# Kernel tuning notes

Hardware: AMD Instinct MI355X
Metric: run time of the kernel (lower is better)

The kernel has to match this reference:

```python
import jax, jax.numpy as jnp
import numpy as np

N, E, IN_DIM, H, D = 50000, 800000, 64, 8, 8
HD = H * D
CLAMP = 5.0


def setup_inputs() -> dict:
    key = jax.random.key(0)
    ks = jax.random.split(key, 13)
    s_in = 1.0 / np.sqrt(IN_DIM)
    s_hd = 1.0 / np.sqrt(HD)
    return {
        "x": jax.random.normal(ks[0], (N, IN_DIM), jnp.float32),
        "edge_attr": jax.random.normal(ks[1], (E, IN_DIM), jnp.float32),
        "edge_index": jax.random.randint(ks[2], (2, E), 0, N, jnp.int32),
        # torch nn.Linear weights are [out_features, in_features]
        "WQ": jax.random.normal(ks[3], (HD, IN_DIM), jnp.float32) * s_in,
        "WK": jax.random.normal(ks[4], (HD, IN_DIM), jnp.float32) * s_in,
        "WV": jax.random.normal(ks[5], (HD, IN_DIM), jnp.float32) * s_in,
        "WEw": jax.random.normal(ks[6], (HD, IN_DIM), jnp.float32) * s_in,
        "WEb": jax.random.normal(ks[7], (HD, IN_DIM), jnp.float32) * s_in,
        "bEb": jax.random.normal(ks[8], (HD,), jnp.float32) * 0.02,
        "WEo": jax.random.normal(ks[9], (HD, HD), jnp.float32) * s_hd,
        "bEo": jax.random.normal(ks[10], (HD,), jnp.float32) * 0.02,
        "Aw": jax.random.normal(ks[11], (D, H, 1), jnp.float32) * s_hd,
        "BW": jax.random.normal(ks[12], (D, H, D), jnp.float32) * s_hd,
    }


def _scatter_softmax(score, dst, num_nodes):
    # score: [E, H, 1]; softmax over edges grouped by dst node
    mx = jax.ops.segment_max(score, dst, num_segments=num_nodes)  # [N,H,1]
    ex = jnp.exp(score - mx[dst])
    den = jax.ops.segment_sum(ex, dst, num_segments=num_nodes)    # [N,H,1]
    return ex / (den[dst] + 1e-16)


def reference(x, edge_attr, edge_index, WQ, WK, WV, WEw, WEb, bEb, WEo, bEo, Aw, BW):
    n = x.shape[0]
    e = edge_attr.shape[0]
    Qh = (x @ WQ.T).reshape(n, H, D)
    Kh = (x @ WK.T).reshape(n, H, D)
    Vh = (x @ WV.T).reshape(n, H, D)
    Ew = (edge_attr @ WEw.T).reshape(e, H, D)
    Eb = (edge_attr @ WEb.T + bEb).reshape(e, H, D)

    dst, src = edge_index[0], edge_index[1]
    conn1 = (Qh[dst] + Kh[src]) * Ew                       # [E,H,D]
    # sqrt(relu(x)) - sqrt(relu(-x)) == sign(x)*sqrt(|x|)
    conn2 = jnp.sign(conn1) * jnp.sqrt(jnp.abs(conn1))
    conn = conn2 + Eb                                      # act = Identity

    Eo_flat = conn.reshape(e, HD) @ WEo.T + bEo            # Oe output [E, H*D]
    Eo = Eo_flat.reshape(e, H, D)

    score = jnp.einsum('ehd,dhc->ehc', conn, Aw)           # [E,H,1]
    score = jnp.clip(score, -CLAMP, CLAMP)
    score = _scatter_softmax(score, dst, n)

    agg = jax.ops.segment_sum(Vh[src] * score, dst, num_segments=n)   # [N,H,D]
    rowV = jax.ops.segment_sum(Eo * score, dst, num_segments=n)       # [N,H,D]
    rowV = jnp.einsum('nhd,dhc->nhc', rowV, BW)
    h_out = agg + rowV                                     # [N,H,D]
    return (h_out, Eo_flat)
```

## Files before the change

kernel.cpp:

```cpp
#include <hip/hip_runtime.h>

#define NN 50000
#define EE 800000
#define NTILES (EE / 128)
#define NB ((NN + 1023) / 1024)

typedef __attribute__((ext_vector_type(8))) short short8;
typedef __attribute__((ext_vector_type(16))) float f32x16;
typedef unsigned short ushort_t;

static __device__ __forceinline__ unsigned short f2bf(float f) {
    unsigned u = __float_as_uint(f);
    u += 0x7fffu + ((u >> 16) & 1u);
    return (unsigned short)(u >> 16);
}
static __device__ __forceinline__ unsigned cvt_pk(float lo, float hi) {
    unsigned r;
    asm("v_cvt_pk_bf16_f32 %0, %1, %2" : "=v"(r) : "v"(lo), "v"(hi));
    return r;
}
static __device__ __forceinline__ float bf2f(unsigned short s) {
    return __uint_as_float((unsigned)s << 16);
}
static __device__ __forceinline__ float lo_f(unsigned u) { return __uint_as_float(u << 16); }
static __device__ __forceinline__ float hi_f(unsigned u) { return __uint_as_float(u & 0xffff0000u); }
static __device__ __forceinline__ f32x16 splat16(float v) {
    f32x16 r;
    #pragma unroll
    for (int i = 0; i < 16; ++i) r[i] = v;
    return r;
}

union U8 { short8 v; uint2 u[2]; };

static __device__ __forceinline__ short8 ldsfrag(const unsigned short* rowbase, int k0) {
    U8 t;
    t.u[0] = *(const uint2*)(rowbase + k0);
    t.u[1] = *(const uint2*)(rowbase + k0 + 8);
    return t.v;
}

__global__ __launch_bounds__(256) void qkv_mfma_kernel(
    const float* __restrict__ x,
    const float* __restrict__ WQ, const float* __restrict__ WK, const float* __restrict__ WV,
    ushort_t* __restrict__ Qb, ushort_t* __restrict__ Kb, ushort_t* __restrict__ Vb)
{
    __shared__ unsigned short s_wq[64][68];
    __shared__ unsigned short s_wk[64][68];
    __shared__ unsigned short s_wv[64][68];

    int tid = threadIdx.x;
    #pragma unroll
    for (int t = 0; t < 8; ++t) {
        int idx = (t * 256 + tid) * 2;
        int r = idx >> 6, c = idx & 63;
        float2 w = *(const float2*)(WQ + idx);
        *(unsigned*)&s_wq[r][c] = cvt_pk(w.x, w.y);
        w = *(const float2*)(WK + idx);
        *(unsigned*)&s_wk[r][c] = cvt_pk(w.x, w.y);
        w = *(const float2*)(WV + idx);
        *(unsigned*)&s_wv[r][c] = cvt_pk(w.x, w.y);
    }
    __syncthreads();

    int wid = tid >> 6, lane = tid & 63;
    int m0 = blockIdx.x * 128 + wid * 32;
    int lo5 = lane & 31, hi = lane >> 5;

    int rowi = m0 + lo5;
    const float* arow = x + (size_t)(rowi < NN ? rowi : NN - 1) * 64;
    short8 af[4];
    #pragma unroll
    for (int ks = 0; ks < 4; ++ks) {
        int k0 = ks * 16 + hi * 4;
        float4 a0 = *(const float4*)(arow + k0);
        float4 a1 = *(const float4*)(arow + k0 + 8);
        U8 t;
        t.u[0] = make_uint2(cvt_pk(a0.x, a0.y), cvt_pk(a0.z, a0.w));
        t.u[1] = make_uint2(cvt_pk(a1.x, a1.y), cvt_pk(a1.z, a1.w));
        af[ks] = t.v;
    }

    #pragma unroll
    for (int nt = 0; nt < 2; ++nt) {
        int n = nt * 32 + lo5;
        f32x16 cQ = splat16(0.f), cK = splat16(0.f), cV = splat16(0.f);
        #pragma unroll
        for (int ks = 0; ks < 4; ++ks) {
            int k0 = ks * 16 + hi * 4;
            cQ = __builtin_amdgcn_mfma_f32_32x32x16_bf16(af[ks], ldsfrag(s_wq[n], k0), cQ, 0, 0, 0);
            cK = __builtin_amdgcn_mfma_f32_32x32x16_bf16(af[ks], ldsfrag(s_wk[n], k0), cK, 0, 0, 0);
            cV = __builtin_amdgcn_mfma_f32_32x32x16_bf16(af[ks], ldsfrag(s_wv[n], k0), cV, 0, 0, 0);
        }
        #pragma unroll
        for (int r = 0; r < 16; ++r) {
            int m = (r & 3) + 8 * (r >> 2) + 4 * hi;
            int gm = m0 + m;
            if (gm < NN) {
                Qb[(size_t)gm * 64 + n] = (ushort_t)cvt_pk(cQ[r], cQ[r]);
                Kb[(size_t)gm * 64 + n] = (ushort_t)cvt_pk(cK[r], cK[r]);
                Vb[(size_t)gm * 64 + n] = (ushort_t)cvt_pk(cV[r], cV[r]);
            }
        }
    }
}

__global__ __launch_bounds__(256) void hist_kernel(const int* __restrict__ eidx,
                                                   int* __restrict__ cnt)
{
    int e = blockIdx.x * blockDim.x + threadIdx.x;
    atomicAdd(&cnt[eidx[e]], 1);
}

__global__ __launch_bounds__(1024) void scan1_kernel(const int* __restrict__ cnt,
                                                     int* __restrict__ rowstart,
                                                     int* __restrict__ bsum)
{
    __shared__ int buf[1024];
    int tid = threadIdx.x;
    int i = blockIdx.x * 1024 + tid;
    int v = (i < NN) ? cnt[i] : 0;
    buf[tid] = v;
    __syncthreads();
    for (int off = 1; off < 1024; off <<= 1) {
        int t = (tid >= off) ? buf[tid - off] : 0;
        __syncthreads();
        buf[tid] += t;
        __syncthreads();
    }
    if (i < NN) rowstart[i] = buf[tid] - v;
    if (tid == 1023) bsum[blockIdx.x] = buf[1023];
}

__global__ __launch_bounds__(64) void scan2_kernel(const int* __restrict__ bsum,
                                                   int* __restrict__ boff,
                                                   int* __restrict__ rowstart)
{
    int lane = threadIdx.x;
    int v = (lane < NB) ? bsum[lane] : 0;
    int s = v;
    #pragma unroll
    for (int off = 1; off < 64; off <<= 1) {
        int t = __shfl_up(s, off, 64);
        if (lane >= off) s += t;
    }
    if (lane < NB) boff[lane] = s - v;
    if (lane == 63) rowstart[NN] = s;
}

__global__ __launch_bounds__(1024) void scan3_kernel(int* __restrict__ rowstart,
                                                     const int* __restrict__ boff,
                                                     int* __restrict__ cursor)
{
    int i = blockIdx.x * 1024 + threadIdx.x;
    if (i < NN) {
        int r = rowstart[i] + boff[blockIdx.x];
        rowstart[i] = r;
        cursor[i] = r;
    }
}

__global__ __launch_bounds__(256) void scatter_kernel(const int* __restrict__ eidx,
                                                      int* __restrict__ cursor,
                                                      int2* __restrict__ edges_csr,
                                                      int* __restrict__ inv)
{
    int e = blockIdx.x * blockDim.x + threadIdx.x;
    int dst = eidx[e];
    int pos = atomicAdd(&cursor[dst], 1);
    edges_csr[pos] = make_int2(e, eidx[EE + e]);
    inv[e] = pos;
}

__global__ __launch_bounds__(256) void edge_mfma_kernel(
    const float* __restrict__ eattr, const int* __restrict__ eidx,
    const int* __restrict__ inv,
    const float* __restrict__ WEw, const float* __restrict__ WEb, const float* __restrict__ bEb,
    const float* __restrict__ WEo, const float* __restrict__ bEo, const float* __restrict__ Aw,
    const ushort_t* __restrict__ Qb, const ushort_t* __restrict__ Kb,
    float* __restrict__ Eo_out, float* __restrict__ exbuf)
{
    __shared__ unsigned short s_wew[64][68];
    __shared__ unsigned short s_web[64][68];
    __shared__ unsigned short s_weo[64][68];
    __shared__ unsigned short s_cq[4][32][68];

    int tid = threadIdx.x;
    #pragma unroll
    for (int t = 0; t < 8; ++t) {
        int idx = (t * 256 + tid) * 2;
        int r = idx >> 6, c = idx & 63;
        float2 w = *(const float2*)(WEw + idx);
        *(unsigned*)&s_wew[r][c] = cvt_pk(w.x, w.y);
        w = *(const float2*)(WEb + idx);
        *(unsigned*)&s_web[r][c] = cvt_pk(w.x, w.y);
        w = *(const float2*)(WEo + idx);
        *(unsigned*)&s_weo[r][c] = cvt_pk(w.x, w.y);
    }
    __syncthreads();

    int wid = tid >> 6, lane = tid & 63;
    int lo5 = lane & 31, hi = lane >> 5;
    int mm = lane >> 4;
    int cc = (lane & 15) * 4;

    float awv[32];
    #pragma unroll
    for (int ks = 0; ks < 4; ++ks)
        #pragma unroll
        for (int i = 0; i < 8; ++i) {
            int k = ks * 16 + hi * 4 + (i & 3) + ((i >> 2) << 3);
            awv[ks * 8 + i] = Aw[(k & 7) * 8 + (k >> 3)];
        }
    float bEbn0 = bEb[lo5], bEbn1 = bEb[32 + lo5];
    float bEon0 = bEo[lo5], bEon1 = bEo[32 + lo5];

    for (int tile = blockIdx.x; tile < NTILES; tile += gridDim.x) {
        int e0 = tile * 128 + wid * 32;
        int pos = inv[e0 + lo5];

        #pragma unroll
        for (int t = 0; t < 8; ++t) {
            int m = t * 4 + mm;
            int e = e0 + m;
            int dst = eidx[e], src = eidx[EE + e];
            uint2 q = *(const uint2*)(Qb + (size_t)dst * 64 + cc);
            uint2 k = *(const uint2*)(Kb + (size_t)src * 64 + cc);
            float s0 = lo_f(q.x) + lo_f(k.x);
            float s1 = hi_f(q.x) + hi_f(k.x);
            float s2 = lo_f(q.y) + lo_f(k.y);
            float s3 = hi_f(q.y) + hi_f(k.y);
            *(uint2*)&s_cq[wid][m][cc] = make_uint2(cvt_pk(s0, s1), cvt_pk(s2, s3));
        }

        short8 af[4];
        {
            const float* arow = eattr + (size_t)(e0 + lo5) * 64;
            #pragma unroll
            for (int ks = 0; ks < 4; ++ks) {
                int k0 = ks * 16 + hi * 4;
                float4 a0 = *(const float4*)(arow + k0);
                float4 a1 = *(const float4*)(arow + k0 + 8);
                U8 t;
                t.u[0] = make_uint2(cvt_pk(a0.x, a0.y), cvt_pk(a0.z, a0.w));
                t.u[1] = make_uint2(cvt_pk(a1.x, a1.y), cvt_pk(a1.z, a1.w));
                af[ks] = t.v;
            }
        }

        #pragma unroll
        for (int nt = 0; nt < 2; ++nt) {
            int n = nt * 32 + lo5;
            f32x16 cEw = splat16(0.f), cEb = splat16(0.f);
            #pragma unroll
            for (int ks = 0; ks < 4; ++ks) {
                int k0 = ks * 16 + hi * 4;
                cEw = __builtin_amdgcn_mfma_f32_32x32x16_bf16(af[ks], ldsfrag(s_wew[n], k0), cEw, 0, 0, 0);
                cEb = __builtin_amdgcn_mfma_f32_32x32x16_bf16(af[ks], ldsfrag(s_web[n], k0), cEb, 0, 0, 0);
            }
            float bEbn = nt ? bEbn1 : bEbn0;
            #pragma unroll
            for (int r = 0; r < 16; ++r) {
                int m = (r & 3) + 8 * (r >> 2) + 4 * hi;
                float qk = bf2f(s_cq[wid][m][n]);
                float c1 = qk * cEw[r];
                float c2 = copysignf(sqrtf(fabsf(c1)), c1);
                s_cq[wid][m][n] = f2bf(c2 + cEb[r] + bEbn);
            }
        }

        short8 ca[4];
        #pragma unroll
        for (int ks = 0; ks < 4; ++ks) {
            int k0 = ks * 16 + hi * 4;
            ca[ks] = ldsfrag(s_cq[wid][lo5], k0);
        }

        {
            float sc[8];
            #pragma unroll
            for (int h2 = 0; h2 < 8; ++h2) sc[h2] = 0.f;
            #pragma unroll
            for (int ks = 0; ks < 4; ++ks)
                #pragma unroll
                for (int i = 0; i < 8; ++i) {
                    float cv = bf2f((unsigned short)ca[ks][i]);
                    sc[2 * ks + (i >> 2)] = fmaf(cv, awv[ks * 8 + i], sc[2 * ks + (i >> 2)]);
                }
            #pragma unroll
            for (int h2 = 0; h2 < 8; ++h2) {
                sc[h2] += __shfl_xor(sc[h2], 32, 64);
                sc[h2] = fminf(fmaxf(sc[h2], -5.0f), 5.0f);
                sc[h2] = __expf(sc[h2]);
            }
            if (hi == 0) {
                *(float4*)(exbuf + (size_t)pos * 8 + 0) = make_float4(sc[0], sc[1], sc[2], sc[3]);
                *(float4*)(exbuf + (size_t)pos * 8 + 4) = make_float4(sc[4], sc[5], sc[6], sc[7]);
            }
        }

        #pragma unroll
        for (int nt = 0; nt < 2; ++nt) {
            int n = nt * 32 + lo5;
            f32x16 cO = splat16(nt ? bEon1 : bEon0);
            #pragma unroll
            for (int ks = 0; ks < 4; ++ks) {
                int k0 = ks * 16 + hi * 4;
                cO = __builtin_amdgcn_mfma_f32_32x32x16_bf16(ca[ks], ldsfrag(s_weo[n], k0), cO, 0, 0, 0);
            }
            #pragma unroll
            for (int r = 0; r < 16; ++r) {
                int m = (r & 3) + 8 * (r >> 2) + 4 * hi;
                Eo_out[(size_t)(e0 + m) * 64 + n] = cO[r];
            }
        }
    }
}

__global__ __launch_bounds__(256) void node_kernel(
    const int* __restrict__ rowstart, const int2* __restrict__ edges_csr,
    const float* __restrict__ exbuf, const float* __restrict__ Eo,
    const ushort_t* __restrict__ Vb, const float* __restrict__ BW,
    float* __restrict__ hout)
{
    int n = (blockIdx.x * blockDim.x + threadIdx.x) >> 6;
    int lane = threadIdx.x & 63;
    int h = lane >> 3, d = lane & 7;

    int beg = rowstart[n], end = rowstart[n + 1];
    float agg0 = 0.f, rv0 = 0.f, den0 = 0.f;
    float agg1 = 0.f, rv1 = 0.f, den1 = 0.f;
    int j = beg;
    for (; j + 3 < end; j += 4) {
        int2 p0 = edges_csr[j + 0];
        int2 p1 = edges_csr[j + 1];
        int2 p2 = edges_csr[j + 2];
        int2 p3 = edges_csr[j + 3];
        float x0 = exbuf[(size_t)(j + 0) * 8 + h];
        float x1 = exbuf[(size_t)(j + 1) * 8 + h];
        float x2 = exbuf[(size_t)(j + 2) * 8 + h];
        float x3 = exbuf[(size_t)(j + 3) * 8 + h];
        float v0 = bf2f(Vb[(size_t)p0.y * 64 + lane]);
        float o0 = Eo[(size_t)p0.x * 64 + lane];
        float v1 = bf2f(Vb[(size_t)p1.y * 64 + lane]);
        float o1 = Eo[(size_t)p1.x * 64 + lane];
        float v2 = bf2f(Vb[(size_t)p2.y * 64 + lane]);
        float o2 = Eo[(size_t)p2.x * 64 + lane];
        float v3 = bf2f(Vb[(size_t)p3.y * 64 + lane]);
        float o3 = Eo[(size_t)p3.x * 64 + lane];
        agg0 = fmaf(x0, v0, agg0); rv0 = fmaf(x0, o0, rv0); den0 += x0;
        agg1 = fmaf(x1, v1, agg1); rv1 = fmaf(x1, o1, rv1); den1 += x1;
        agg0 = fmaf(x2, v2, agg0); rv0 = fmaf(x2, o2, rv0); den0 += x2;
        agg1 = fmaf(x3, v3, agg1); rv1 = fmaf(x3, o3, rv1); den1 += x3;
    }
    for (; j < end; ++j) {
        int2 p0 = edges_csr[j];
        float x0 = exbuf[(size_t)j * 8 + h];
        agg0 = fmaf(x0, bf2f(Vb[(size_t)p0.y * 64 + lane]), agg0);
        rv0  = fmaf(x0, Eo[(size_t)p0.x * 64 + lane], rv0);
        den0 += x0;
    }
    float agg = agg0 + agg1, rv = rv0 + rv1, den = den0 + den1;
    float inv = (den > 0.f) ? (1.0f / den) : 0.f;

    float acc = agg;
    #pragma unroll
    for (int dd = 0; dd < 8; ++dd) {
        float rvd = __shfl(rv, (h << 3) + dd, 64);
        acc = fmaf(rvd, BW[dd * 64 + (h << 3) + d], acc);
    }
    hout[(size_t)n * 64 + lane] = acc * inv;
}

extern "C" void kernel_launch(void* const* d_in, const int* in_sizes, int n_in,
                              void* d_out, int out_size, void* d_ws, size_t ws_size,
                              hipStream_t stream)
{
    const float* x    = (const float*)d_in[0];
    const float* ea   = (const float*)d_in[1];
    const int*   eidx = (const int*)  d_in[2];
    const float* WQ   = (const float*)d_in[3];
    const float* WK   = (const float*)d_in[4];
    const float* WV   = (const float*)d_in[5];
    const float* WEw  = (const float*)d_in[6];
    const float* WEb  = (const float*)d_in[7];
    const float* bEb  = (const float*)d_in[8];
    const float* WEo  = (const float*)d_in[9];
    const float* bEo  = (const float*)d_in[10];
    const float* Aw   = (const float*)d_in[11];
    const float* BW   = (const float*)d_in[12];

    float* hout   = (float*)d_out;
    float* Eo_out = hout + (size_t)NN * 64;

    ushort_t* Qb = (ushort_t*)d_ws;
    ushort_t* Kb = Qb + (size_t)NN * 64;
    ushort_t* Vb = Kb + (size_t)NN * 64;
    float* exbuf = (float*)(Vb + (size_t)NN * 64);
    int* cnt      = (int*)(exbuf + (size_t)EE * 8);
    int* rowstart = cnt + NN;
    int2* edges_csr = (int2*)(rowstart + NN + 2);
    int* invp     = (int*)(edges_csr + EE);
    int* bsum     = invp + EE;
    int* boff     = bsum + 64;

    hipMemsetAsync(cnt, 0, (size_t)NN * sizeof(int), stream);

    hist_kernel<<<EE / 256, 256, 0, stream>>>(eidx, cnt);
    scan1_kernel<<<NB, 1024, 0, stream>>>(cnt, rowstart, bsum);
    scan2_kernel<<<1, 64, 0, stream>>>(bsum, boff, rowstart);
    scan3_kernel<<<NB, 1024, 0, stream>>>(rowstart, boff, cnt);
    scatter_kernel<<<EE / 256, 256, 0, stream>>>(eidx, cnt, edges_csr, invp);

    qkv_mfma_kernel<<<(NN + 127) / 128, 256, 0, stream>>>(x, WQ, WK, WV, Qb, Kb, Vb);

    edge_mfma_kernel<<<2080, 256, 0, stream>>>(ea, eidx, invp, WEw, WEb, bEb,
                                               WEo, bEo, Aw, Qb, Kb, Eo_out, exbuf);

    node_kernel<<<(NN * 64) / 256, 256, 0, stream>>>(rowstart, edges_csr,
                                                     exbuf, Eo_out, Vb, BW, hout);
}
```

Before: 318.7 us.

## Write bf16 Eo copy in CSR order so node kernel reads it contiguously

The edge kernel now also writes a bf16 copy of Eo, permuted into destination-sorted CSR order, into extra workspace. The node kernel then reads this copy contiguously instead of gathering fp32 Eo rows by edge id. The aim is to replace a random 256B-per-edge gather with a sequential 128B read. The cost is an extra scattered 2-byte-per-element write in the edge kernel, which is poorly coalesced, plus bf16 rounding in the rowV path. A fallback path is used when the workspace is too small, and there the node kernel's unroll drops from 4 to 2.

```diff
diff --git a/kernel.cpp b/kernel.cpp
--- a/kernel.cpp
+++ b/kernel.cpp
@@ -172,18 +172,21 @@
     inv[e] = pos;
 }
 
+template<bool WCSR>
 __global__ __launch_bounds__(256) void edge_mfma_kernel(
     const float* __restrict__ eattr, const int* __restrict__ eidx,
     const int* __restrict__ inv,
     const float* __restrict__ WEw, const float* __restrict__ WEb, const float* __restrict__ bEb,
     const float* __restrict__ WEo, const float* __restrict__ bEo, const float* __restrict__ Aw,
     const ushort_t* __restrict__ Qb, const ushort_t* __restrict__ Kb,
-    float* __restrict__ Eo_out, float* __restrict__ exbuf)
+    float* __restrict__ Eo_out, float* __restrict__ exbuf,
+    ushort_t* __restrict__ eocsr)
 {
     __shared__ unsigned short s_wew[64][68];
     __shared__ unsigned short s_web[64][68];
     __shared__ unsigned short s_weo[64][68];
     __shared__ unsigned short s_cq[4][32][68];
+    __shared__ int s_inv[4][32];
 
     int tid = threadIdx.x;
     #pragma unroll
@@ -218,6 +221,7 @@
     for (int tile = blockIdx.x; tile < NTILES; tile += gridDim.x) {
         int e0 = tile * 128 + wid * 32;
         int pos = inv[e0 + lo5];
+        if (WCSR) s_inv[wid][lo5] = pos;
 
         #pragma unroll
         for (int t = 0; t < 8; ++t) {
@@ -312,14 +316,18 @@
             for (int r = 0; r < 16; ++r) {
                 int m = (r & 3) + 8 * (r >> 2) + 4 * hi;
                 Eo_out[(size_t)(e0 + m) * 64 + n] = cO[r];
-            }
-        }
-    }
-}
-
-__global__ __launch_bounds__(256) void node_kernel(
+                if (WCSR) {
+                    int pm = s_inv[wid][m];
+                    eocsr[(size_t)pm * 64 + n] = (ushort_t)cvt_pk(cO[r], cO[r]);
+                }
+            }
+        }
+    }
+}
+
+__global__ __launch_bounds__(256) void node_kernel_csr(
     const int* __restrict__ rowstart, const int2* __restrict__ edges_csr,
-    const float* __restrict__ exbuf, const float* __restrict__ Eo,
+    const float* __restrict__ exbuf, const ushort_t* __restrict__ eocsr,
     const ushort_t* __restrict__ Vb, const float* __restrict__ BW,
     float* __restrict__ hout)
 {
@@ -341,19 +349,64 @@
         float x2 = exbuf[(size_t)(j + 2) * 8 + h];
         float x3 = exbuf[(size_t)(j + 3) * 8 + h];
         float v0 = bf2f(Vb[(size_t)p0.y * 64 + lane]);
-        float o0 = Eo[(size_t)p0.x * 64 + lane];
+        float o0 = bf2f(eocsr[(size_t)(j + 0) * 64 + lane]);
         float v1 = bf2f(Vb[(size_t)p1.y * 64 + lane]);
-        float o1 = Eo[(size_t)p1.x * 64 + lane];
+        float o1 = bf2f(eocsr[(size_t)(j + 1) * 64 + lane]);
         float v2 = bf2f(Vb[(size_t)p2.y * 64 + lane]);
-        float o2 = Eo[(size_t)p2.x * 64 + lane];
+        float o2 = bf2f(eocsr[(size_t)(j + 2) * 64 + lane]);
         float v3 = bf2f(Vb[(size_t)p3.y * 64 + lane]);
-        float o3 = Eo[(size_t)p3.x * 64 + lane];
+        float o3 = bf2f(eocsr[(size_t)(j + 3) * 64 + lane]);
         agg0 = fmaf(x0, v0, agg0); rv0 = fmaf(x0, o0, rv0); den0 += x0;
         agg1 = fmaf(x1, v1, agg1); rv1 = fmaf(x1, o1, rv1); den1 += x1;
         agg0 = fmaf(x2, v2, agg0); rv0 = fmaf(x2, o2, rv0); den0 += x2;
         agg1 = fmaf(x3, v3, agg1); rv1 = fmaf(x3, o3, rv1); den1 += x3;
     }
     for (; j < end; ++j) {
+        int2 p0 = edges_csr[j];
+        float x0 = exbuf[(size_t)j * 8 + h];
+        agg0 = fmaf(x0, bf2f(Vb[(size_t)p0.y * 64 + lane]), agg0);
+        rv0  = fmaf(x0, bf2f(eocsr[(size_t)j * 64 + lane]), rv0);
+        den0 += x0;
+    }
+    float agg = agg0 + agg1, rv = rv0 + rv1, den = den0 + den1;
+    float inv = (den > 0.f) ? (1.0f / den) : 0.f;
+
+    float acc = agg;
+    #pragma unroll
+    for (int dd = 0; dd < 8; ++dd) {
+        float rvd = __shfl(rv, (h << 3) + dd, 64);
+        acc = fmaf(rvd, BW[dd * 64 + (h << 3) + d], acc);
+    }
+    hout[(size_t)n * 64 + lane] = acc * inv;
+}
+
+__global__ __launch_bounds__(256) void node_kernel_f32(
+    const int* __restrict__ rowstart, const int2* __restrict__ edges_csr,
+    const float* __restrict__ exbuf, const float* __restrict__ Eo,
+    const ushort_t* __restrict__ Vb, const float* __restrict__ BW,
+    float* __restrict__ hout)
+{
+    int n = (blockIdx.x * blockDim.x + threadIdx.x) >> 6;
+    int lane = threadIdx.x & 63;
+    int h = lane >> 3, d = lane & 7;
+
+    int beg = rowstart[n], end = rowstart[n + 1];
+    float agg0 = 0.f, rv0 = 0.f, den0 = 0.f;
+    float agg1 = 0.f, rv1 = 0.f, den1 = 0.f;
+    int j = beg;
+    for (; j + 1 < end; j += 2) {
+        int2 p0 = edges_csr[j + 0];
+        int2 p1 = edges_csr[j + 1];
+        float x0 = exbuf[(size_t)(j + 0) * 8 + h];
+        float x1 = exbuf[(size_t)(j + 1) * 8 + h];
+        agg0 = fmaf(x0, bf2f(Vb[(size_t)p0.y * 64 + lane]), agg0);
+        rv0  = fmaf(x0, Eo[(size_t)p0.x * 64 + lane], rv0);
+        den0 += x0;
+        agg1 = fmaf(x1, bf2f(Vb[(size_t)p1.y * 64 + lane]), agg1);
+        rv1  = fmaf(x1, Eo[(size_t)p1.x * 64 + lane], rv1);
+        den1 += x1;
+    }
+    if (j < end) {
         int2 p0 = edges_csr[j];
         float x0 = exbuf[(size_t)j * 8 + h];
         agg0 = fmaf(x0, bf2f(Vb[(size_t)p0.y * 64 + lane]), agg0);
@@ -403,6 +456,9 @@
     int* invp     = (int*)(edges_csr + EE);
     int* bsum     = invp + EE;
     int* boff     = bsum + 64;
+    ushort_t* eocsr = (ushort_t*)(boff + 64);
+    size_t need = (size_t)((char*)(eocsr + (size_t)EE * 64) - (char*)d_ws);
+    bool use_csr = (ws_size >= need);
 
     hipMemsetAsync(cnt, 0, (size_t)NN * sizeof(int), stream);
 
@@ -414,9 +470,17 @@
 
     qkv_mfma_kernel<<<(NN + 127) / 128, 256, 0, stream>>>(x, WQ, WK, WV, Qb, Kb, Vb);
 
-    edge_mfma_kernel<<<2080, 256, 0, stream>>>(ea, eidx, invp, WEw, WEb, bEb,
-                                               WEo, bEo, Aw, Qb, Kb, Eo_out, exbuf);
-
-    node_kernel<<<(NN * 64) / 256, 256, 0, stream>>>(rowstart, edges_csr,
-                                                     exbuf, Eo_out, Vb, BW, hout);
-}
+    if (use_csr) {
+        edge_mfma_kernel<true><<<2080, 256, 0, stream>>>(ea, eidx, invp, WEw, WEb, bEb,
+                                                         WEo, bEo, Aw, Qb, Kb,
+                                                         Eo_out, exbuf, eocsr);
+        node_kernel_csr<<<(NN * 64) / 256, 256, 0, stream>>>(rowstart, edges_csr,
+                                                             exbuf, eocsr, Vb, BW, hout);
+    } else {
+        edge_mfma_kernel<false><<<2080, 256, 0, stream>>>(ea, eidx, invp, WEw, WEb, bEb,
+                                                          WEo, bEo, Aw, Qb, Kb,
+                                                          Eo_out, exbuf, eocsr);
+        node_kernel_f32<<<(NN * 64) / 256, 256, 0, stream>>>(rowstart, edges_csr,
+                                                             exbuf, Eo_out, Vb, BW, hout);
+    }
+}
```

Result: slower. 389.0 us (+22.0%).
